# Performance work log

Measured on AMD Instinct MI355X. Metric: run time of the kernel, lower is better.

The kernel has to match this reference:

```python
import jax, jax.numpy as jnp
import numpy as np

HIDDEN = 2048
NUM_HEADS = 16
NUM_KV_HEADS = 8
HEAD_DIM = 128
EPS = 1e-6
ROPE_THETA = 10000.0
T = 2048
Q_SIZE = NUM_HEADS * HEAD_DIM          # 2048
KV_SIZE = NUM_KV_HEADS * HEAD_DIM      # 1024


def setup_inputs() -> dict:
    key = jax.random.key(0)
    k1, k2, k3, k4, k5 = jax.random.split(key, 5)
    positions = jnp.arange(T, dtype=jnp.int32)
    hidden_states = jax.random.normal(k1, (T, HIDDEN), dtype=jnp.float32)
    s = 0.02
    qkv_w = jax.random.normal(k2, (Q_SIZE + 2 * KV_SIZE, HIDDEN), dtype=jnp.float32) * s
    o_w = jax.random.normal(k3, (HIDDEN, Q_SIZE), dtype=jnp.float32) * s
    q_norm_w = jnp.ones((HEAD_DIM,), dtype=jnp.float32) + 0.1 * jax.random.normal(k4, (HEAD_DIM,), dtype=jnp.float32)
    k_norm_w = jnp.ones((HEAD_DIM,), dtype=jnp.float32) + 0.1 * jax.random.normal(k5, (HEAD_DIM,), dtype=jnp.float32)
    return {"positions": positions, "hidden_states": hidden_states,
            "qkv_w": qkv_w, "q_norm_w": q_norm_w, "k_norm_w": k_norm_w, "o_w": o_w}


def _rms_norm(x, w):
    # x: [T, H, D], normalize over last dim
    var = jnp.mean(x * x, axis=-1, keepdims=True)
    return x * jax.lax.rsqrt(var + EPS) * w


def _rope(x, positions):
    # neox-style rotary over full head_dim; x: [T, H, D]
    half = HEAD_DIM // 2
    inv_freq = 1.0 / (ROPE_THETA ** (jnp.arange(0, half, dtype=jnp.float32) / half))
    freqs = positions.astype(jnp.float32)[:, None] * inv_freq  # [T, D/2]
    cos = jnp.cos(freqs)[:, None, :]  # [T, 1, D/2]
    sin = jnp.sin(freqs)[:, None, :]
    x1, x2 = x[..., :half], x[..., half:]
    return jnp.concatenate([x1 * cos - x2 * sin, x2 * cos + x1 * sin], axis=-1)


def reference(positions, hidden_states, qkv_w, q_norm_w, k_norm_w, o_w):
    G = NUM_HEADS // NUM_KV_HEADS  # query groups per kv head
    scale = HEAD_DIM ** -0.5
    qkv = hidden_states @ qkv_w.T  # [T, Q+2KV]
    q, k, v = jnp.split(qkv, [Q_SIZE, Q_SIZE + KV_SIZE], axis=-1)
    q = q.reshape(T, NUM_HEADS, HEAD_DIM)
    k = k.reshape(T, NUM_KV_HEADS, HEAD_DIM)
    v = v.reshape(T, NUM_KV_HEADS, HEAD_DIM)
    # qkv_bias=False path -> per-head RMSNorm on q and k
    q = _rms_norm(q, q_norm_w)
    k = _rms_norm(k, k_norm_w)
    q = _rope(q, positions)
    k = _rope(k, positions)
    # GQA causal attention
    qg = q.reshape(T, NUM_KV_HEADS, G, HEAD_DIM)
    scores = jnp.einsum('qkgd,skd->kgqs', qg, k) * scale  # [KV, G, T, T]
    causal = positions[:, None] >= positions[None, :]  # [T, T]
    scores = jnp.where(causal, scores, jnp.finfo(scores.dtype).min)
    probs = jax.nn.softmax(scores, axis=-1)
    ctx = jnp.einsum('kgqs,skd->qkgd', probs, v)  # [T, KV, G, D]
    ctx = ctx.reshape(T, Q_SIZE)
    return ctx @ o_w.T  # [T, HIDDEN]
```

## Files before the change

kernel.cpp:

```cpp
#include <hip/hip_runtime.h>
#include <math.h>

#define T_SEQ     2048
#define HIDDEN_   2048
#define NUM_HEADS 16
#define NUM_KV    8
#define HEAD_DIM  128
#define Q_SIZE    2048
#define KV_SIZE   1024
#define QKV_N     4096
#define QK_N      3072
#define EPS_      1e-6f

typedef __attribute__((ext_vector_type(8))) short short8;
typedef __attribute__((ext_vector_type(4))) float floatx4;

__device__ __forceinline__ unsigned short f2bf(float f) {
    unsigned int u = __float_as_uint(f);
    u += 0x7fffu + ((u >> 16) & 1u);
    return (unsigned short)(u >> 16);
}
__device__ __forceinline__ float b2f(unsigned short u) {
    return __uint_as_float((unsigned int)u << 16);
}

__device__ __forceinline__ void stage16(const unsigned short* g, unsigned short* lds_base) {
    __builtin_amdgcn_global_load_lds(
        (const __attribute__((address_space(1))) unsigned int*)g,
        (__attribute__((address_space(3))) unsigned int*)lds_base, 16, 0, 0);
}

#define H4 (T_SEQ * HIDDEN_ / 4)
#define W4 (QKV_N * HIDDEN_ / 4)
#define O4 (Q_SIZE * HIDDEN_ / 4)

__global__ __launch_bounds__(256) void convert_all(
    const float* __restrict__ hidden, const float* __restrict__ qkv_w,
    const float* __restrict__ o_w, unsigned short* __restrict__ hbf,
    unsigned short* __restrict__ wbf, unsigned short* __restrict__ obf)
{
    int i = blockIdx.x * 256 + threadIdx.x;
    const float4* src;
    ushort4* dst;
    int j;
    if (i < H4)            { src = (const float4*)hidden; dst = (ushort4*)hbf; j = i; }
    else if (i < H4 + W4)  { src = (const float4*)qkv_w;  dst = (ushort4*)wbf; j = i - H4; }
    else                   { src = (const float4*)o_w;    dst = (ushort4*)obf; j = i - H4 - W4;
                             if (j >= O4) return; }
    float4 v = src[j];
    ushort4 o;
    o.x = f2bf(v.x); o.y = f2bf(v.y); o.z = f2bf(v.z); o.w = f2bf(v.w);
    dst[j] = o;
}

template<int MODE>
__global__ __launch_bounds__(512, 4) void gemm_nt_bf16(
    const unsigned short* __restrict__ A, const unsigned short* __restrict__ B,
    float* __restrict__ C,
    unsigned short* __restrict__ Qb, unsigned short* __restrict__ Kb,
    unsigned short* __restrict__ Vt,
    const int* __restrict__ positions,
    const float* __restrict__ qw, const float* __restrict__ kw,
    int M, int N, int K)
{
    __shared__ unsigned short smem[32768];
    unsigned short* const As0 = smem;
    unsigned short* const Bs0 = smem + 16384;

    const int tid  = threadIdx.x;
    const int w    = tid >> 6;
    const int lane = tid & 63;
    const int colL = lane & 15;
    const int quad = lane >> 4;
    const int bm = blockIdx.y * 128;
    const int bn = blockIdx.x * 128;
    const int wm = (w >> 2) * 64;
    const int wn = (w & 3) * 32;

    floatx4 acc[4][2];
    #pragma unroll
    for (int i = 0; i < 4; ++i)
        #pragma unroll
        for (int j = 0; j < 2; ++j)
            acc[i][j] = (floatx4){0.f, 0.f, 0.f, 0.f};

    int s_r[2], s_lc[2];
    #pragma unroll
    for (int cc = 0; cc < 2; ++cc) {
        int s = cc * 512 + tid;
        int r = s >> 3, pc = s & 7;
        s_r[cc] = r;
        s_lc[cc] = pc ^ (r & 7);
    }

    auto stage_tile = [&](int buf, int k0) {
        unsigned short* la = As0 + buf * 8192;
        unsigned short* lb = Bs0 + buf * 8192;
        #pragma unroll
        for (int cc = 0; cc < 2; ++cc) {
            stage16(A + (size_t)(bm + s_r[cc]) * K + k0 + s_lc[cc] * 8,
                    la + (cc * 512 + w * 64) * 8);
            stage16(B + (size_t)(bn + s_r[cc]) * K + k0 + s_lc[cc] * 8,
                    lb + (cc * 512 + w * 64) * 8);
        }
    };

    const int nt = K >> 6;
    stage_tile(0, 0);

    for (int t = 0; t < nt; ++t) {
        const int b = t & 1;
        if (t + 1 < nt) {
            stage_tile(b ^ 1, (t + 1) << 6);
            asm volatile("s_waitcnt vmcnt(4)" ::: "memory");
        } else {
            asm volatile("s_waitcnt vmcnt(0)" ::: "memory");
        }
        __builtin_amdgcn_s_barrier();
        __builtin_amdgcn_sched_barrier(0);

        const unsigned short* la = As0 + b * 8192;
        const unsigned short* lb = Bs0 + b * 8192;
        #pragma unroll
        for (int kk = 0; kk < 2; ++kk) {
            short8 af[4], bfv[2];
            #pragma unroll
            for (int i = 0; i < 4; ++i) {
                int ra = wm + i * 16 + colL;
                af[i]  = *(const short8*)&la[ra * 64 + (((kk * 4 + quad) ^ (ra & 7)) * 8)];
            }
            #pragma unroll
            for (int j = 0; j < 2; ++j) {
                int rb = wn + j * 16 + colL;
                bfv[j] = *(const short8*)&lb[rb * 64 + (((kk * 4 + quad) ^ (rb & 7)) * 8)];
            }
            #pragma unroll
            for (int i = 0; i < 4; ++i)
                #pragma unroll
                for (int j = 0; j < 2; ++j)
                    acc[i][j] = __builtin_amdgcn_mfma_f32_16x16x32_bf16(af[i], bfv[j], acc[i][j], 0, 0, 0);
        }
        __builtin_amdgcn_sched_barrier(0);
        asm volatile("" ::: "memory");
        __builtin_amdgcn_s_barrier();
    }

    if constexpr (MODE == 0) {
        #pragma unroll
        for (int i = 0; i < 4; ++i)
            #pragma unroll
            for (int j = 0; j < 2; ++j)
                #pragma unroll
                for (int rr = 0; rr < 4; ++rr) {
                    int row = bm + wm + i * 16 + quad * 4 + rr;
                    int cc2 = bn + wn + j * 16 + colL;
                    C[(size_t)row * N + cc2] = acc[i][j][rr];
                }
    } else {
        if (bn < QK_N) {
            __shared__ float sums[4][128];
            unsigned short* xnL = smem;

            float p[4][4];
            #pragma unroll
            for (int i = 0; i < 4; ++i)
                #pragma unroll
                for (int rr = 0; rr < 4; ++rr) {
                    float s = 0.f;
                    #pragma unroll
                    for (int j = 0; j < 2; ++j)
                        s = fmaf(acc[i][j][rr], acc[i][j][rr], s);
                    p[i][rr] = s;
                }
            #pragma unroll
            for (int off = 1; off < 16; off <<= 1)
                #pragma unroll
                for (int i = 0; i < 4; ++i)
                    #pragma unroll
                    for (int rr = 0; rr < 4; ++rr)
                        p[i][rr] += __shfl_xor(p[i][rr], off, 64);
            if (colL == 0) {
                #pragma unroll
                for (int i = 0; i < 4; ++i)
                    #pragma unroll
                    for (int rr = 0; rr < 4; ++rr)
                        sums[w & 3][wm + i * 16 + quad * 4 + rr] = p[i][rr];
            }
            __syncthreads();

            float inv_r[4][4];
            #pragma unroll
            for (int i = 0; i < 4; ++i)
                #pragma unroll
                for (int rr = 0; rr < 4; ++rr) {
                    int row = wm + i * 16 + quad * 4 + rr;
                    float tot = (sums[0][row] + sums[1][row]) + (sums[2][row] + sums[3][row]);
                    inv_r[i][rr] = rsqrtf(tot * (1.0f / HEAD_DIM) + EPS_);
                }

            const float* nw = (bn < Q_SIZE) ? qw : kw;
            float wv[2];
            #pragma unroll
            for (int j = 0; j < 2; ++j)
                wv[j] = nw[wn + j * 16 + colL];

            #pragma unroll
            for (int i = 0; i < 4; ++i)
                #pragma unroll
                for (int j = 0; j < 2; ++j) {
                    ushort4 pk;
                    pk.x = f2bf(acc[i][j][0] * inv_r[i][0] * wv[j]);
                    pk.y = f2bf(acc[i][j][1] * inv_r[i][1] * wv[j]);
                    pk.z = f2bf(acc[i][j][2] * inv_r[i][2] * wv[j]);
                    pk.w = f2bf(acc[i][j][3] * inv_r[i][3] * wv[j]);
                    int d = wn + j * 16 + colL;
                    *(ushort4*)&xnL[d * 132 + wm + i * 16 + quad * 4] = pk;
                }
            __syncthreads();
            {
                const int r = tid >> 2;
                const int qd = tid & 3;
                const float pos = (float)positions[bm + r];
                const bool is_q = (bn < Q_SIZE);
                const float l2r = 13.287712379549449f / 64.0f;
                const float sc = 0.08838834764831845f;
                unsigned short* rowp;
                if (is_q) rowp = Qb + (size_t)(bm + r) * Q_SIZE + (bn >> 7) * HEAD_DIM;
                else      rowp = Kb + ((size_t)((bn - Q_SIZE) >> 7) * T_SEQ + bm + r) * HEAD_DIM;

                #pragma unroll
                for (int f4 = 0; f4 < 16; f4 += 4) {
                    ushort4 lo, hi;
                    #pragma unroll
                    for (int e = 0; e < 4; ++e) {
                        int f = qd * 16 + f4 + e;
                        float x1 = b2f(xnL[f * 132 + r]);
                        float x2 = b2f(xnL[(f + 64) * 132 + r]);
                        float s, c;
                        __sincosf(pos * exp2f(-(float)f * l2r), &s, &c);
                        float olo = fmaf(x1, c, -x2 * s);
                        float ohi = fmaf(x2, c,  x1 * s);
                        if (is_q) { olo *= sc; ohi *= sc; }
                        ((unsigned short*)&lo)[e] = f2bf(olo);
                        ((unsigned short*)&hi)[e] = f2bf(ohi);
                    }
                    *(ushort4*)(rowp + qd * 16 + f4)      = lo;
                    *(ushort4*)(rowp + 64 + qd * 16 + f4) = hi;
                }
            }
        } else {
            const int kvh = (bn - QK_N) >> 7;
            #pragma unroll
            for (int i = 0; i < 4; ++i)
                #pragma unroll
                for (int j = 0; j < 2; ++j) {
                    int d = wn + j * 16 + colL;
                    int tok = bm + wm + i * 16 + quad * 4;
                    ushort4 o;
                    o.x = f2bf(acc[i][j][0]); o.y = f2bf(acc[i][j][1]);
                    o.z = f2bf(acc[i][j][2]); o.w = f2bf(acc[i][j][3]);
                    *(ushort4*)&Vt[((size_t)kvh * HEAD_DIM + d) * T_SEQ + tok] = o;
                }
        }
    }
}

#define BQ 64
#define BK 32

__global__ __launch_bounds__(256) void attn_mfma(
    const unsigned short* __restrict__ Qb, const unsigned short* __restrict__ Kb,
    const unsigned short* __restrict__ Vt, unsigned short* __restrict__ ctxb,
    float* __restrict__ partO, float* __restrict__ partL)
{
    const int h = blockIdx.y;
    int qt, ch;
    {
        int x = blockIdx.x;
        if (x < 16) { qt = 16 + x; ch = 0; }
        else {
            int p = (x - 16) >> 1;
            if (((x - 16) & 1) == 0) { qt = 15 - p; ch = 0; }
            else                     { qt = 31 - p; ch = 1; }
        }
    }
    const int nch = (qt >= 16) ? 2 : 1;
    const int units = (ch == 0) ? ((qt + 1 < 16) ? 2 * (qt + 1) : 32)
                                : (2 * (qt + 1) - 32);
    const int q0 = qt * BQ;
    const int kv = h >> 1;
    const int tid = threadIdx.x;
    const int w = tid >> 6;
    const int lane = tid & 63;
    const int col = lane & 15;
    const int quad = lane >> 4;

    __shared__ unsigned short Ks[2][32 * 128];
    __shared__ unsigned short Vs[2][144 * 32];
    __shared__ unsigned short Ps[4][16][40];

    {
        int x = tid * 2;
        unsigned short vv = (x < 32) ? (unsigned short)0x3F80 : (unsigned short)0;
        ushort2 o = {vv, vv};
        *(ushort2*)&Vs[0][128 * 32 + x] = o;
        *(ushort2*)&Vs[1][128 * 32 + x] = o;
    }

    short8 qf[4];
    {
        const unsigned short* qp = Qb + (size_t)(q0 + w * 16 + col) * Q_SIZE + h * HEAD_DIM;
        #pragma unroll
        for (int c = 0; c < 4; ++c)
            qf[c] = *(const short8*)(qp + c * 32 + quad * 8);
    }

    const unsigned short* kg[2];
    const unsigned short* vg[2];
    #pragma unroll
    for (int it = 0; it < 2; ++it) {
        int s = it * 256 + tid;
        int kr = s >> 4, kp = s & 15, kj = kp ^ (kr & 15);
        kg[it] = Kb + (size_t)kv * T_SEQ * HEAD_DIM + kr * HEAD_DIM + kj * 8;
        int vr = s >> 2, vp = s & 3, vj = vp ^ ((vr >> 1) & 3);
        vg[it] = Vt + (size_t)kv * HEAD_DIM * T_SEQ + (size_t)vr * T_SEQ + vj * 8;
    }

    floatx4 Ob[9];
    #pragma unroll
    for (int cb = 0; cb < 9; ++cb) Ob[cb] = (floatx4){0.f, 0.f, 0.f, 0.f};

    const int wave_qmin = q0 + w * 16;
    const int wave_qmax = wave_qmin + 15;
    const int tok_base = ch * 1024;

    #pragma unroll
    for (int it = 0; it < 2; ++it) {
        stage16(kg[it] + (size_t)tok_base * HEAD_DIM, &Ks[0][(it * 256 + w * 64) * 8]);
        stage16(vg[it] + tok_base, &Vs[0][(it * 256 + w * 64) * 8]);
    }

    for (int u = 0; u < units; ++u) {
        const int t0 = tok_base + u * BK;
        __syncthreads();
        if (u + 1 < units) {
            const int tn = t0 + BK;
            const int b = (u + 1) & 1;
            #pragma unroll
            for (int it = 0; it < 2; ++it) {
                stage16(kg[it] + (size_t)tn * HEAD_DIM, &Ks[b][(it * 256 + w * 64) * 8]);
                stage16(vg[it] + tn, &Vs[b][(it * 256 + w * 64) * 8]);
            }
        }
        if (t0 > wave_qmax) continue;
        const unsigned short* ks = Ks[u & 1];
        const unsigned short* vs = Vs[u & 1];

        floatx4 S[2];
        #pragma unroll
        for (int cb = 0; cb < 2; ++cb) {
            floatx4 a = (floatx4){0.f, 0.f, 0.f, 0.f};
            #pragma unroll
            for (int c = 0; c < 4; ++c) {
                short8 kf = *(const short8*)&ks[((cb * 16 + col) * 16 + ((c * 4 + quad) ^ col)) * 8];
                a = __builtin_amdgcn_mfma_f32_16x16x32_bf16(kf, qf[c], a, 0, 0, 0);
            }
            S[cb] = a;
        }

        const int qr = q0 + w * 16 + col;
        if (t0 + 31 <= wave_qmin) {
            #pragma unroll
            for (int cb = 0; cb < 2; ++cb) {
                ushort4 pk;
                pk.x = f2bf(__expf(S[cb][0])); pk.y = f2bf(__expf(S[cb][1]));
                pk.z = f2bf(__expf(S[cb][2])); pk.w = f2bf(__expf(S[cb][3]));
                *(ushort4*)&Ps[w][col][cb * 16 + quad * 4] = pk;
            }
        } else {
            #pragma unroll
            for (int cb = 0; cb < 2; ++cb) {
                int kt = t0 + cb * 16 + quad * 4;
                ushort4 pk;
                pk.x = (kt + 0 <= qr) ? f2bf(__expf(S[cb][0])) : (unsigned short)0;
                pk.y = (kt + 1 <= qr) ? f2bf(__expf(S[cb][1])) : (unsigned short)0;
                pk.z = (kt + 2 <= qr) ? f2bf(__expf(S[cb][2])) : (unsigned short)0;
                pk.w = (kt + 3 <= qr) ? f2bf(__expf(S[cb][3])) : (unsigned short)0;
                *(ushort4*)&Ps[w][col][cb * 16 + quad * 4] = pk;
            }
        }

        short8 pf = *(const short8*)&Ps[w][col][quad * 8];
        #pragma unroll
        for (int cb = 0; cb < 9; ++cb) {
            int vrow = cb * 16 + col;
            short8 vf = *(const short8*)&vs[(vrow * 4 + (quad ^ ((vrow >> 1) & 3))) * 8];
            Ob[cb] = __builtin_amdgcn_mfma_f32_16x16x32_bf16(pf, vf, Ob[cb], 0, 0, 0);
        }
    }

    if (nch == 1) {
        #pragma unroll
        for (int r = 0; r < 4; ++r) {
            float l = __shfl(Ob[8][r], lane & 48);
            float rl = 1.0f / l;
            const int qrow = q0 + w * 16 + quad * 4 + r;
            #pragma unroll
            for (int cb = 0; cb < 8; ++cb)
                ctxb[(size_t)qrow * Q_SIZE + h * HEAD_DIM + cb * 16 + col] = f2bf(Ob[cb][r] * rl);
        }
    } else {
        const int slot = (h * 16 + (qt - 16)) * 2 + ch;
        float* po = partO + (size_t)slot * (BQ * HEAD_DIM);
        #pragma unroll
        for (int cb = 0; cb < 8; ++cb)
            #pragma unroll
            for (int r = 0; r < 4; ++r)
                po[(w * 16 + quad * 4 + r) * HEAD_DIM + cb * 16 + col] = Ob[cb][r];
        if (col == 0) {
            #pragma unroll
            for (int r = 0; r < 4; ++r)
                partL[slot * BQ + w * 16 + quad * 4 + r] = Ob[8][r];
        }
    }
}

__global__ __launch_bounds__(256) void combine(
    const float* __restrict__ partO, const float* __restrict__ partL,
    unsigned short* __restrict__ ctxb)
{
    const int h = blockIdx.x >> 4;
    const int qi = blockIdx.x & 15;
    const int q0 = (16 + qi) * 64;
    const int slot0 = (h * 16 + qi) * 2;
    const int tid = threadIdx.x;
    const int row = tid >> 2;
    const int seg = tid & 3;

    const float l = partL[slot0 * 64 + row] + partL[(slot0 + 1) * 64 + row];
    const float rl = 1.0f / l;
    const float* p0 = partO + (size_t)slot0 * 8192 + row * 128 + seg * 32;
    const float* p1 = p0 + 8192;
    unsigned short* dst = ctxb + (size_t)(q0 + row) * Q_SIZE + h * HEAD_DIM + seg * 32;
    #pragma unroll
    for (int m = 0; m < 8; ++m) {
        float4 a = *(const float4*)(p0 + m * 4);
        float4 b = *(const float4*)(p1 + m * 4);
        ushort4 o;
        o.x = f2bf((a.x + b.x) * rl); o.y = f2bf((a.y + b.y) * rl);
        o.z = f2bf((a.z + b.z) * rl); o.w = f2bf((a.w + b.w) * rl);
        *(ushort4*)(dst + m * 4) = o;
    }
}

extern "C" void kernel_launch(void* const* d_in, const int* in_sizes, int n_in,
                              void* d_out, int out_size, void* d_ws, size_t ws_size,
                              hipStream_t stream)
{
    const int*   positions = (const int*)d_in[0];
    const float* hidden    = (const float*)d_in[1];
    const float* qkv_w     = (const float*)d_in[2];
    const float* q_norm_w  = (const float*)d_in[3];
    const float* k_norm_w  = (const float*)d_in[4];
    const float* o_w       = (const float*)d_in[5];
    float* out = (float*)d_out;

    const size_t MB = 1024 * 1024;
    char* ws = (char*)d_ws;
    unsigned short* obf  = (unsigned short*)ws;
    unsigned short* hbf  = (unsigned short*)(ws + 8 * MB);
    unsigned short* wbf  = (unsigned short*)(ws + 16 * MB);
    unsigned short* Vt   = (unsigned short*)(ws + 32 * MB);
    unsigned short* Qb   = (unsigned short*)(ws + 36 * MB);
    unsigned short* Kb   = (unsigned short*)(ws + 44 * MB);
    unsigned short* ctxb = (unsigned short*)(ws + 48 * MB);
    float* partL         = (float*)(ws + 8 * MB);
    float* partO         = (float*)(ws + 16 * MB);

    convert_all<<<(H4 + W4 + O4 + 255) / 256, 256, 0, stream>>>(
        hidden, qkv_w, o_w, hbf, wbf, obf);
    gemm_nt_bf16<1><<<dim3(QKV_N / 128, T_SEQ / 128), 512, 0, stream>>>(
        hbf, wbf, nullptr, Qb, Kb, Vt, positions, q_norm_w, k_norm_w,
        T_SEQ, QKV_N, HIDDEN_);
    attn_mfma<<<dim3(48, NUM_HEADS), 256, 0, stream>>>(Qb, Kb, Vt, ctxb, partO, partL);
    combine<<<256, 256, 0, stream>>>(partO, partL, ctxb);
    gemm_nt_bf16<0><<<dim3(Q_SIZE / 128, T_SEQ / 128), 512, 0, stream>>>(
        ctxb, obf, out, nullptr, nullptr, nullptr, nullptr, nullptr, nullptr,
        T_SEQ, Q_SIZE, HIDDEN_);
}
```

Before: 223.0 us.

## Split K across warp pairs in GEMM with 64x64 warp tiles and LDS reduction

The 8 warps of each GEMM block are regrouped into 4 spatial 64x64 tiles, with two warps per tile each handling half of the 64-wide K slice (intra-K split). Each warp now loads 4 A and 4 B fragments per K tile for 16 MFMAs, instead of looping over two k-substeps with 4x2 fragments, which raises MFMA-per-LDS-read reuse. After the main loop, partner warps exchange half of their accumulators through shared memory and sum them, so every warp ends up with a 64x32 output slice for the existing epilogues. This costs twice the accumulator registers, which may lower occupancy, plus an extra LDS exchange and barrier.

```diff
diff --git a/kernel.cpp b/kernel.cpp
--- a/kernel.cpp
+++ b/kernel.cpp
@@ -74,21 +74,24 @@
     const int quad = lane >> 4;
     const int bm = blockIdx.y * 128;
     const int bn = blockIdx.x * 128;
-    const int wm = (w >> 2) * 64;
-    const int wn = (w & 3) * 32;
-
-    floatx4 acc[4][2];
+    const int s  = w & 3;
+    const int ks = w >> 2;
+    const int wm = (s & 1) * 64;
+    const int wn = (s >> 1) * 64;
+    const int wnE = wn + ks * 32;
+
+    floatx4 acc[4][4];
     #pragma unroll
     for (int i = 0; i < 4; ++i)
         #pragma unroll
-        for (int j = 0; j < 2; ++j)
+        for (int j = 0; j < 4; ++j)
             acc[i][j] = (floatx4){0.f, 0.f, 0.f, 0.f};
 
     int s_r[2], s_lc[2];
     #pragma unroll
     for (int cc = 0; cc < 2; ++cc) {
-        int s = cc * 512 + tid;
-        int r = s >> 3, pc = s & 7;
+        int ss = cc * 512 + tid;
+        int r = ss >> 3, pc = ss & 7;
         s_r[cc] = r;
         s_lc[cc] = pc ^ (r & 7);
     }
@@ -121,56 +124,87 @@
 
         const unsigned short* la = As0 + b * 8192;
         const unsigned short* lb = Bs0 + b * 8192;
-        #pragma unroll
-        for (int kk = 0; kk < 2; ++kk) {
-            short8 af[4], bfv[2];
-            #pragma unroll
-            for (int i = 0; i < 4; ++i) {
-                int ra = wm + i * 16 + colL;
-                af[i]  = *(const short8*)&la[ra * 64 + (((kk * 4 + quad) ^ (ra & 7)) * 8)];
-            }
-            #pragma unroll
-            for (int j = 0; j < 2; ++j) {
-                int rb = wn + j * 16 + colL;
-                bfv[j] = *(const short8*)&lb[rb * 64 + (((kk * 4 + quad) ^ (rb & 7)) * 8)];
-            }
-            #pragma unroll
-            for (int i = 0; i < 4; ++i)
-                #pragma unroll
-                for (int j = 0; j < 2; ++j)
-                    acc[i][j] = __builtin_amdgcn_mfma_f32_16x16x32_bf16(af[i], bfv[j], acc[i][j], 0, 0, 0);
-        }
+        short8 af[4], bfv[4];
+        #pragma unroll
+        for (int i = 0; i < 4; ++i) {
+            int ra = wm + i * 16 + colL;
+            af[i]  = *(const short8*)&la[ra * 64 + (((ks * 4 + quad) ^ (ra & 7)) * 8)];
+        }
+        #pragma unroll
+        for (int j = 0; j < 4; ++j) {
+            int rb = wn + j * 16 + colL;
+            bfv[j] = *(const short8*)&lb[rb * 64 + (((ks * 4 + quad) ^ (rb & 7)) * 8)];
+        }
+        #pragma unroll
+        for (int i = 0; i < 4; ++i)
+            #pragma unroll
+            for (int j = 0; j < 4; ++j)
+                acc[i][j] = __builtin_amdgcn_mfma_f32_16x16x32_bf16(af[i], bfv[j], acc[i][j], 0, 0, 0);
         __builtin_amdgcn_sched_barrier(0);
         asm volatile("" ::: "memory");
         __builtin_amdgcn_s_barrier();
     }
 
+    floatx4* exch = (floatx4*)smem;
+    if (ks == 0) {
+        #pragma unroll
+        for (int i = 0; i < 4; ++i)
+            #pragma unroll
+            for (int jj = 0; jj < 2; ++jj)
+                exch[((w * 4 + i) * 2 + jj) * 64 + lane] = acc[i][2 + jj];
+    } else {
+        #pragma unroll
+        for (int i = 0; i < 4; ++i)
+            #pragma unroll
+            for (int jj = 0; jj < 2; ++jj)
+                exch[((w * 4 + i) * 2 + jj) * 64 + lane] = acc[i][jj];
+    }
+    __syncthreads();
+    floatx4 accR[4][2];
+    {
+        const int pw = w ^ 4;
+        if (ks == 0) {
+            #pragma unroll
+            for (int i = 0; i < 4; ++i)
+                #pragma unroll
+                for (int jj = 0; jj < 2; ++jj)
+                    accR[i][jj] = acc[i][jj] + exch[((pw * 4 + i) * 2 + jj) * 64 + lane];
+        } else {
+            #pragma unroll
+            for (int i = 0; i < 4; ++i)
+                #pragma unroll
+                for (int jj = 0; jj < 2; ++jj)
+                    accR[i][jj] = acc[i][2 + jj] + exch[((pw * 4 + i) * 2 + jj) * 64 + lane];
+        }
+    }
+
     if constexpr (MODE == 0) {
         #pragma unroll
         for (int i = 0; i < 4; ++i)
             #pragma unroll
-            for (int j = 0; j < 2; ++j)
+            for (int jj = 0; jj < 2; ++jj)
                 #pragma unroll
                 for (int rr = 0; rr < 4; ++rr) {
                     int row = bm + wm + i * 16 + quad * 4 + rr;
-                    int cc2 = bn + wn + j * 16 + colL;
-                    C[(size_t)row * N + cc2] = acc[i][j][rr];
+                    int cc2 = bn + wnE + jj * 16 + colL;
+                    C[(size_t)row * N + cc2] = accR[i][jj][rr];
                 }
     } else {
         if (bn < QK_N) {
             __shared__ float sums[4][128];
             unsigned short* xnL = smem;
+            const int g = ((w >> 1) & 1) * 2 + ks;
 
             float p[4][4];
             #pragma unroll
             for (int i = 0; i < 4; ++i)
                 #pragma unroll
                 for (int rr = 0; rr < 4; ++rr) {
-                    float s = 0.f;
+                    float sv = 0.f;
                     #pragma unroll
-                    for (int j = 0; j < 2; ++j)
-                        s = fmaf(acc[i][j][rr], acc[i][j][rr], s);
-                    p[i][rr] = s;
+                    for (int jj = 0; jj < 2; ++jj)
+                        sv = fmaf(accR[i][jj][rr], accR[i][jj][rr], sv);
+                    p[i][rr] = sv;
                 }
             #pragma unroll
             for (int off = 1; off < 16; off <<= 1)
@@ -184,7 +218,7 @@
                 for (int i = 0; i < 4; ++i)
                     #pragma unroll
                     for (int rr = 0; rr < 4; ++rr)
-                        sums[w & 3][wm + i * 16 + quad * 4 + rr] = p[i][rr];
+                        sums[g][wm + i * 16 + quad * 4 + rr] = p[i][rr];
             }
             __syncthreads();
 
@@ -201,19 +235,19 @@
             const float* nw = (bn < Q_SIZE) ? qw : kw;
             float wv[2];
             #pragma unroll
-            for (int j = 0; j < 2; ++j)
-                wv[j] = nw[wn + j * 16 + colL];
+            for (int jj = 0; jj < 2; ++jj)
+                wv[jj] = nw[wnE + jj * 16 + colL];
 
             #pragma unroll
             for (int i = 0; i < 4; ++i)
                 #pragma unroll
-                for (int j = 0; j < 2; ++j) {
+                for (int jj = 0; jj < 2; ++jj) {
                     ushort4 pk;
-                    pk.x = f2bf(acc[i][j][0] * inv_r[i][0] * wv[j]);
-                    pk.y = f2bf(acc[i][j][1] * inv_r[i][1] * wv[j]);
-                    pk.z = f2bf(acc[i][j][2] * inv_r[i][2] * wv[j]);
-                    pk.w = f2bf(acc[i][j][3] * inv_r[i][3] * wv[j]);
-                    int d = wn + j * 16 + colL;
+                    pk.x = f2bf(accR[i][jj][0] * inv_r[i][0] * wv[jj]);
+                    pk.y = f2bf(accR[i][jj][1] * inv_r[i][1] * wv[jj]);
+                    pk.z = f2bf(accR[i][jj][2] * inv_r[i][2] * wv[jj]);
+                    pk.w = f2bf(accR[i][jj][3] * inv_r[i][3] * wv[jj]);
+                    int d = wnE + jj * 16 + colL;
                     *(ushort4*)&xnL[d * 132 + wm + i * 16 + quad * 4] = pk;
                 }
             __syncthreads();
@@ -236,10 +270,10 @@
                         int f = qd * 16 + f4 + e;
                         float x1 = b2f(xnL[f * 132 + r]);
                         float x2 = b2f(xnL[(f + 64) * 132 + r]);
-                        float s, c;
-                        __sincosf(pos * exp2f(-(float)f * l2r), &s, &c);
-                        float olo = fmaf(x1, c, -x2 * s);
-                        float ohi = fmaf(x2, c,  x1 * s);
+                        float sv, cv;
+                        __sincosf(pos * exp2f(-(float)f * l2r), &sv, &cv);
+                        float olo = fmaf(x1, cv, -x2 * sv);
+                        float ohi = fmaf(x2, cv,  x1 * sv);
                         if (is_q) { olo *= sc; ohi *= sc; }
                         ((unsigned short*)&lo)[e] = f2bf(olo);
                         ((unsigned short*)&hi)[e] = f2bf(ohi);
@@ -253,12 +287,12 @@
             #pragma unroll
             for (int i = 0; i < 4; ++i)
                 #pragma unroll
-                for (int j = 0; j < 2; ++j) {
-                    int d = wn + j * 16 + colL;
+                for (int jj = 0; jj < 2; ++jj) {
+                    int d = wnE + jj * 16 + colL;
                     int tok = bm + wm + i * 16 + quad * 4;
                     ushort4 o;
-                    o.x = f2bf(acc[i][j][0]); o.y = f2bf(acc[i][j][1]);
-                    o.z = f2bf(acc[i][j][2]); o.w = f2bf(acc[i][j][3]);
+                    o.x = f2bf(accR[i][jj][0]); o.y = f2bf(accR[i][jj][1]);
+                    o.z = f2bf(accR[i][jj][2]); o.w = f2bf(accR[i][jj][3]);
                     *(ushort4*)&Vt[((size_t)kvh * HEAD_DIM + d) * T_SEQ + tok] = o;
                 }
         }
```

Measured after the change: 226.8 us. No clear change (+1.7%).
